# Performance work log

Measured on AMD Instinct MI355X. Metric: run time of the kernel, lower is better.

## Reference

```python
import jax, jax.numpy as jnp
import numpy as np

B, L, D, H = 64, 2048, 512, 8
DH = D // H


def setup_inputs() -> dict:
    key = jax.random.key(0)
    ks = jax.random.split(key, 8)
    Q = jax.random.normal(ks[0], (B, 1, D), dtype=jnp.float32)
    K = jax.random.normal(ks[1], (B, L, D), dtype=jnp.float32)
    s = 1.0 / np.sqrt(D)
    Ww = jax.random.uniform(ks[2], (D, D), jnp.float32, -s, s)
    Wb = jax.random.uniform(ks[3], (D,), jnp.float32, -s, s)
    Uw = jax.random.uniform(ks[4], (D, D), jnp.float32, -s, s)
    Ub = jax.random.uniform(ks[5], (D,), jnp.float32, -s, s)
    sv = 1.0 / np.sqrt(DH)
    Vw = jax.random.uniform(ks[6], (DH,), jnp.float32, -sv, sv)
    Vb = jax.random.uniform(ks[7], (1,), jnp.float32, -sv, sv)
    return {"Q": Q, "K": K, "Ww": Ww, "Wb": Wb, "Uw": Uw, "Ub": Ub, "Vw": Vw, "Vb": Vb}


def reference(Q, K, Ww, Wb, Uw, Ub, Vw, Vb):
    b, l, d = K.shape
    lq = Q.shape[1]
    # torch Linear: x @ W.T + b
    Wq = (Q @ Ww.T + Wb).reshape(b, H, lq, DH)   # raw reshape, matches torch
    Uk = (K @ Uw.T + Ub).reshape(b, H, l, DH)    # raw reshape (splits L axis)
    # V: Linear(DH -> 1) applied to tanh(W + U) -> [b, H, l]
    score = jnp.tanh(Wq + Uk) @ Vw + Vb[0]       # [b, H, l]
    score = score[:, :, None, :]                  # squeeze(-1).unsqueeze(2) -> [b, H, 1, l]
    dist = jax.nn.softmax(score, axis=-1)         # softmax over sequence
    Kh = K.reshape(b, H, l, DH)                   # raw reshape, matches torch
    attn = jnp.einsum('bhql,bhld->bhqd', dist, Kh)  # [b, H, 1, DH]
    attn = attn.reshape(b, 1, H * DH)             # [b, 1, D]
    return attn, dist
```

## Files before the change

kernel.cpp:

```cpp
#include <hip/hip_runtime.h>

typedef _Float16 h8_t __attribute__((ext_vector_type(8)));
typedef _Float16 h4_t __attribute__((ext_vector_type(4)));
typedef float f32x4 __attribute__((ext_vector_type(4)));

#define NB 64
#define NH 8
#define NL 2048
#define ND 512

#define GLD_LDS16(g, l) \
    __builtin_amdgcn_global_load_lds((const __attribute__((address_space(1))) unsigned int*)(g), \
                                     (__attribute__((address_space(3))) unsigned int*)(l), 16, 0, 0)

__device__ __forceinline__ int swz_idx(int row, int chunk) {
    return row * 32 + ((chunk ^ ((row >> 1) & 3)) << 3);
}

__global__ __launch_bounds__(256) void wq_kernel(const float* __restrict__ Q,
                                                 const float* __restrict__ Ww,
                                                 const float* __restrict__ Wb,
                                                 float* __restrict__ Wq) {
    __shared__ float q[ND];
    const int b = blockIdx.x;
    const int t = threadIdx.x;
    for (int i = t; i < ND; i += 256) q[i] = Q[b * ND + i];
    __syncthreads();
    for (int j = t; j < ND; j += 256) {
        const float* wr = Ww + (size_t)j * ND;
        float acc = 0.f;
        for (int k = 0; k < ND; k += 4) {
            float4 w = *(const float4*)(wr + k);
            acc += q[k] * w.x + q[k + 1] * w.y + q[k + 2] * w.z + q[k + 3] * w.w;
        }
        Wq[b * ND + j] = acc + Wb[j];
    }
}

__global__ __launch_bounds__(256) void cvt_uw_kernel(const float* __restrict__ Uw,
                                                     _Float16* __restrict__ UwH) {
    const size_t i = ((size_t)blockIdx.x * 256 + threadIdx.x) * 4;
    float4 v = *(const float4*)(Uw + i);
    h4_t h = {(_Float16)v.x, (_Float16)v.y, (_Float16)v.z, (_Float16)v.w};
    *(h4_t*)(UwH + i) = h;
}

__global__ __launch_bounds__(512, 4) void uk_score_kernel(
    const float* __restrict__ Km,
    const _Float16* __restrict__ UwH,
    const float* __restrict__ Ub,
    const float* __restrict__ Wq,
    const float* __restrict__ Vw,
    const float* __restrict__ Vb,
    float* __restrict__ scores)
{
    __shared__ __align__(16) _Float16 Al[2][128 * 32];
    __shared__ __align__(16) _Float16 Bl[2][256 * 32];

    const int t = threadIdx.x;
    const int lane = t & 63;
    const int wave = t >> 6;
    const int wm = wave >> 2;
    const int wn = wave & 3;

    const int bid = blockIdx.x;
    const int swz = (bid & 7) * 256 + (bid >> 3);
    const int tn = swz & 1;
    const int tm = swz >> 1;
    const size_t row0 = (size_t)tm * 128;
    const int n0 = tn * 256;

    f32x4 acc[4][4];
#pragma unroll
    for (int i = 0; i < 4; ++i)
#pragma unroll
        for (int j = 0; j < 4; ++j) acc[i][j] = (f32x4){0.f, 0.f, 0.f, 0.f};

    const int arow = t >> 2;
    const int achunk = t & 3;
    const float* gA = Km + (row0 + arow) * (size_t)ND + achunk * 8;
    const int a_dst = swz_idx(arow, achunk);

    const int brow0 = t >> 2;
    const int bc0 = (t & 3) ^ ((brow0 >> 1) & 3);
    const int brow1 = (512 + t) >> 2;
    const int bc1 = (t & 3) ^ ((brow1 >> 1) & 3);
    const _Float16* gB0 = UwH + (size_t)(n0 + brow0) * ND + bc0 * 8;
    const _Float16* gB1 = UwH + (size_t)(n0 + brow1) * ND + bc1 * 8;
    const int bdst0 = (t & ~63) * 16;
    const int bdst1 = (512 + (t & ~63)) * 16;

    const int col16 = lane & 15;
    const int kg = lane >> 4;

    GLD_LDS16(gB0, (char*)Bl[0] + bdst0);
    GLD_LDS16(gB1, (char*)Bl[0] + bdst1);
    {
        float4 v0 = *(const float4*)(gA);
        float4 v1 = *(const float4*)(gA + 4);
        h8_t ah = {(_Float16)v0.x, (_Float16)v0.y, (_Float16)v0.z, (_Float16)v0.w,
                   (_Float16)v1.x, (_Float16)v1.y, (_Float16)v1.z, (_Float16)v1.w};
        *(h8_t*)&Al[0][a_dst] = ah;
    }
    __syncthreads();

    for (int ks = 0; ks < 16; ++ks) {
        const int cur = ks & 1;
        const int nxt = cur ^ 1;
        const int kk = ks * 32;

        float4 v0n, v1n;
        if (ks < 15) {
            GLD_LDS16(gB0 + kk + 32, (char*)Bl[nxt] + bdst0);
            GLD_LDS16(gB1 + kk + 32, (char*)Bl[nxt] + bdst1);
            v0n = *(const float4*)(gA + kk + 32);
            v1n = *(const float4*)(gA + kk + 36);
        }

        h8_t af[4], bf[4];
#pragma unroll
        for (int i = 0; i < 4; ++i)
            af[i] = *(const h8_t*)&Al[cur][swz_idx(wm * 64 + i * 16 + col16, kg)];
#pragma unroll
        for (int j = 0; j < 4; ++j)
            bf[j] = *(const h8_t*)&Bl[cur][swz_idx(wn * 64 + j * 16 + col16, kg)];
#pragma unroll
        for (int i = 0; i < 4; ++i)
#pragma unroll
            for (int j = 0; j < 4; ++j)
                acc[i][j] = __builtin_amdgcn_mfma_f32_16x16x32_f16(af[i], bf[j], acc[i][j], 0, 0, 0);

        if (ks < 15) {
            h8_t ah = {(_Float16)v0n.x, (_Float16)v0n.y, (_Float16)v0n.z, (_Float16)v0n.w,
                       (_Float16)v1n.x, (_Float16)v1n.y, (_Float16)v1n.z, (_Float16)v1n.w};
            *(h8_t*)&Al[nxt][a_dst] = ah;
        }
        __syncthreads();
    }

    const int b = (int)(row0 >> 11);
    const int h = ((int)row0 >> 8) & 7;
    const int i256b = (int)row0 & 255;

    float vw[4], wqv[4], ubv[4];
#pragma unroll
    for (int j = 0; j < 4; ++j) {
        const int jglob = n0 + wn * 64 + j * 16 + col16;
        const int dh = jglob & 63;
        vw[j] = Vw[dh];
        wqv[j] = Wq[b * ND + h * 64 + dh];
        ubv[j] = Ub[jglob];
    }
    const float vb0 = Vb[0];
    const int jb = tn * 4 + wn;
    const int bh = b * 8 + h;

#pragma unroll
    for (int i = 0; i < 4; ++i) {
#pragma unroll
        for (int r = 0; r < 4; ++r) {
            float s = 0.f;
#pragma unroll
            for (int j = 0; j < 4; ++j) {
                float x = acc[i][j][r] + wqv[j] + ubv[j];
                x = fminf(fmaxf(x, -15.f), 15.f);
                float e = __expf(2.f * x);
                s += ((e - 1.f) / (e + 1.f)) * vw[j];
            }
#pragma unroll
            for (int o = 8; o >= 1; o >>= 1) s += __shfl_xor(s, o);
            if (col16 == 0) {
                const int rloc = wm * 64 + i * 16 + (lane >> 4) * 4 + r;
                const int m = (i256b + rloc) * 8 + jb;
                scores[(size_t)bh * NL + m] = s + vb0;
            }
        }
    }
}

__global__ __launch_bounds__(256) void softmax_attn_kernel(
    const float* __restrict__ Km,
    const float* __restrict__ scores,
    float* __restrict__ out)
{
    __shared__ float sd[NL];
    __shared__ float red[256];
    __shared__ float att[16][64];

    const int bh = blockIdx.x;
    const int b = bh >> 3, h = bh & 7;
    const int t = threadIdx.x;

    float loc[8];
    float mx = -1e30f;
#pragma unroll
    for (int j = 0; j < 8; ++j) {
        loc[j] = scores[(size_t)bh * NL + j * 256 + t];
        mx = fmaxf(mx, loc[j]);
    }
    red[t] = mx;
    __syncthreads();
    for (int s2 = 128; s2 > 0; s2 >>= 1) {
        if (t < s2) red[t] = fmaxf(red[t], red[t + s2]);
        __syncthreads();
    }
    mx = red[0];
    __syncthreads();
    float sum = 0.f;
#pragma unroll
    for (int j = 0; j < 8; ++j) {
        loc[j] = __expf(loc[j] - mx);
        sum += loc[j];
    }
    red[t] = sum;
    __syncthreads();
    for (int s2 = 128; s2 > 0; s2 >>= 1) {
        if (t < s2) red[t] += red[t + s2];
        __syncthreads();
    }
    const float inv = 1.f / red[0];
    __syncthreads();

    float* dist_out = out + 32768 + (size_t)bh * NL;
#pragma unroll
    for (int j = 0; j < 8; ++j) {
        float d = loc[j] * inv;
        sd[j * 256 + t] = d;
        dist_out[j * 256 + t] = d;
    }
    __syncthreads();

    const int wave = t >> 6, lane = t & 63;
    const int g = lane >> 4;
    const int c4 = (lane & 15) * 4;
    f32x4 acc = (f32x4){0.f, 0.f, 0.f, 0.f};
    const float* kb = Km + ((size_t)b * NL + h * 256) * ND;
    for (int rr = 0; rr < 16; ++rr) {
        const int row = wave * 64 + rr * 4 + g;
        const float* kr = kb + (size_t)row * ND;
#pragma unroll
        for (int jb2 = 0; jb2 < 8; ++jb2) {
            const float w = sd[row * 8 + jb2];
            float4 v = *(const float4*)(kr + jb2 * 64 + c4);
            acc[0] += w * v.x;
            acc[1] += w * v.y;
            acc[2] += w * v.z;
            acc[3] += w * v.w;
        }
    }
    *(f32x4*)&att[wave * 4 + g][c4] = acc;
    __syncthreads();
    if (t < 64) {
        float a = 0.f;
#pragma unroll
        for (int i = 0; i < 16; ++i) a += att[i][t];
        out[(size_t)b * ND + h * 64 + t] = a;
    }
}

extern "C" void kernel_launch(void* const* d_in, const int* in_sizes, int n_in,
                              void* d_out, int out_size, void* d_ws, size_t ws_size,
                              hipStream_t stream) {
    const float* Q  = (const float*)d_in[0];
    const float* Km = (const float*)d_in[1];
    const float* Ww = (const float*)d_in[2];
    const float* Wb = (const float*)d_in[3];
    const float* Uw = (const float*)d_in[4];
    const float* Ub = (const float*)d_in[5];
    const float* Vw = (const float*)d_in[6];
    const float* Vb = (const float*)d_in[7];
    float* out = (float*)d_out;

    char* ws = (char*)d_ws;
    float* scores = (float*)ws;
    float* Wq = (float*)(ws + 4194304);
    _Float16* UwH = (_Float16*)(ws + 4194304 + 131072);

    wq_kernel<<<dim3(64), dim3(256), 0, stream>>>(Q, Ww, Wb, Wq);
    cvt_uw_kernel<<<dim3(256), dim3(256), 0, stream>>>(Uw, UwH);
    uk_score_kernel<<<dim3(2048), dim3(512), 0, stream>>>(Km, UwH, Ub, Wq, Vw, Vb, scores);
    softmax_attn_kernel<<<dim3(512), dim3(256), 0, stream>>>(Km, scores, out);
}
```

Before: 196.8 us.

## Deepen GEMM K-loop software pipeline with register A prefetch and manual waitcnts

Restructures the projection GEMM main loop so the fp32 K tile is prefetched into registers two steps ahead, while the fp16 Uw tile keeps its one-step-ahead global-to-LDS load. The loop is fully unrolled, and explicit s_waitcnt and sched_barrier calls order the loads, MFMAs and the single workgroup barrier per step. The aim is to hide global load latency behind the MFMA work and stop the compiler from reordering memory operations. The cost is more registers and fragile hand-written vmcnt accounting that has to match the exact number of loads in flight.

```diff
diff --git a/kernel.cpp b/kernel.cpp
--- a/kernel.cpp
+++ b/kernel.cpp
@@ -12,6 +12,7 @@
 #define GLD_LDS16(g, l) \
     __builtin_amdgcn_global_load_lds((const __attribute__((address_space(1))) unsigned int*)(g), \
                                      (__attribute__((address_space(3))) unsigned int*)(l), 16, 0, 0)
+#define SBAR() __builtin_amdgcn_sched_barrier(0)
 
 __device__ __forceinline__ int swz_idx(int row, int chunk) {
     return row * 32 + ((chunk ^ ((row >> 1) & 3)) << 3);
@@ -93,30 +94,39 @@
     const int col16 = lane & 15;
     const int kg = lane >> 4;
 
-    GLD_LDS16(gB0, (char*)Bl[0] + bdst0);
-    GLD_LDS16(gB1, (char*)Bl[0] + bdst1);
+    float4 rA[2][2];
+
     {
-        float4 v0 = *(const float4*)(gA);
-        float4 v1 = *(const float4*)(gA + 4);
-        h8_t ah = {(_Float16)v0.x, (_Float16)v0.y, (_Float16)v0.z, (_Float16)v0.w,
-                   (_Float16)v1.x, (_Float16)v1.y, (_Float16)v1.z, (_Float16)v1.w};
+        float4 p0 = *(const float4*)(gA);
+        float4 p1 = *(const float4*)(gA + 4);
+        SBAR();
+        GLD_LDS16(gB0, (char*)Bl[0] + bdst0);
+        GLD_LDS16(gB1, (char*)Bl[0] + bdst1);
+        SBAR();
+        rA[1][0] = *(const float4*)(gA + 32);
+        rA[1][1] = *(const float4*)(gA + 36);
+        SBAR();
+        h8_t ah = {(_Float16)p0.x, (_Float16)p0.y, (_Float16)p0.z, (_Float16)p0.w,
+                   (_Float16)p1.x, (_Float16)p1.y, (_Float16)p1.z, (_Float16)p1.w};
         *(h8_t*)&Al[0][a_dst] = ah;
     }
-    __syncthreads();
-
-    for (int ks = 0; ks < 16; ++ks) {
-        const int cur = ks & 1;
-        const int nxt = cur ^ 1;
-        const int kk = ks * 32;
-
-        float4 v0n, v1n;
-        if (ks < 15) {
-            GLD_LDS16(gB0 + kk + 32, (char*)Bl[nxt] + bdst0);
-            GLD_LDS16(gB1 + kk + 32, (char*)Bl[nxt] + bdst1);
-            v0n = *(const float4*)(gA + kk + 32);
-            v1n = *(const float4*)(gA + kk + 36);
-        }
-
+    asm volatile("s_waitcnt vmcnt(2)" ::: "memory");
+    asm volatile("s_waitcnt lgkmcnt(0)" ::: "memory");
+    SBAR();
+    __builtin_amdgcn_s_barrier();
+    SBAR();
+    GLD_LDS16(gB0 + 32, (char*)Bl[1] + bdst0);
+    GLD_LDS16(gB1 + 32, (char*)Bl[1] + bdst1);
+    SBAR();
+
+#pragma unroll
+    for (int s = 0; s < 16; ++s) {
+        const int cur = s & 1;
+        if (s <= 13) {
+            rA[cur][0] = *(const float4*)(gA + (s + 2) * 32);
+            rA[cur][1] = *(const float4*)(gA + (s + 2) * 32 + 4);
+        }
+        SBAR();
         h8_t af[4], bf[4];
 #pragma unroll
         for (int i = 0; i < 4; ++i)
@@ -124,18 +134,33 @@
 #pragma unroll
         for (int j = 0; j < 4; ++j)
             bf[j] = *(const h8_t*)&Bl[cur][swz_idx(wn * 64 + j * 16 + col16, kg)];
+        asm volatile("s_waitcnt lgkmcnt(0)" ::: "memory");
+        SBAR();
 #pragma unroll
         for (int i = 0; i < 4; ++i)
 #pragma unroll
             for (int j = 0; j < 4; ++j)
                 acc[i][j] = __builtin_amdgcn_mfma_f32_16x16x32_f16(af[i], bf[j], acc[i][j], 0, 0, 0);
-
-        if (ks < 15) {
-            h8_t ah = {(_Float16)v0n.x, (_Float16)v0n.y, (_Float16)v0n.z, (_Float16)v0n.w,
-                       (_Float16)v1n.x, (_Float16)v1n.y, (_Float16)v1n.z, (_Float16)v1n.w};
-            *(h8_t*)&Al[nxt][a_dst] = ah;
-        }
-        __syncthreads();
+        SBAR();
+        if (s <= 14) {
+            if (s == 14) { asm volatile("s_waitcnt vmcnt(0)" ::: "memory"); }
+            else         { asm volatile("s_waitcnt vmcnt(2)" ::: "memory"); }
+            SBAR();
+            const float4 q0 = rA[cur ^ 1][0];
+            const float4 q1 = rA[cur ^ 1][1];
+            h8_t ah = {(_Float16)q0.x, (_Float16)q0.y, (_Float16)q0.z, (_Float16)q0.w,
+                       (_Float16)q1.x, (_Float16)q1.y, (_Float16)q1.z, (_Float16)q1.w};
+            *(h8_t*)&Al[cur ^ 1][a_dst] = ah;
+            asm volatile("s_waitcnt lgkmcnt(0)" ::: "memory");
+            SBAR();
+            __builtin_amdgcn_s_barrier();
+            SBAR();
+            if (s <= 13) {
+                GLD_LDS16(gB0 + (s + 2) * 32, (char*)Bl[cur] + bdst0);
+                GLD_LDS16(gB1 + (s + 2) * 32, (char*)Bl[cur] + bdst1);
+            }
+            SBAR();
+        }
     }
 
     const int b = (int)(row0 >> 11);
@@ -170,7 +195,7 @@
 #pragma unroll
             for (int o = 8; o >= 1; o >>= 1) s += __shfl_xor(s, o);
             if (col16 == 0) {
-                const int rloc = wm * 64 + i * 16 + (lane >> 4) * 4 + r;
+                const int rloc = wm * 64 + i * 16 + kg * 4 + r;
                 const int m = (i256b + rloc) * 8 + jb;
                 scores[(size_t)bh * NL + m] = s + vb0;
             }
```

New measurement: 195.9 us. Within noise of the previous version (-0.5%).
